# Kernel tuning notes

Hardware: AMD Instinct MI355X
Metric: run time of the kernel (lower is better)

The kernel has to match this reference:

```python
import jax, jax.numpy as jnp
import numpy as np

N_HEAD = 16


def setup_inputs() -> dict:
    key = jax.random.key(0)
    k0, k1, k2, k3 = jax.random.split(key, 4)
    B, T, C = 2, 2048, 1024
    scale = 0.02
    x = jax.random.normal(k0, (B, T, C), dtype=jnp.float32)
    W_attn = jax.random.normal(k1, (C, 3 * C), dtype=jnp.float32) * scale
    b_attn = jnp.zeros((3 * C,), dtype=jnp.float32)
    W_proj = jax.random.normal(k2, (C, C), dtype=jnp.float32) * scale
    b_proj = jnp.zeros((C,), dtype=jnp.float32)
    return {"x": x, "W_attn": W_attn, "b_attn": b_attn, "W_proj": W_proj, "b_proj": b_proj}


def reference(x, W_attn, b_attn, W_proj, b_proj):
    B, T, C = x.shape
    H = N_HEAD
    hd = C // H
    # fused qkv projection
    qkv = x @ W_attn + b_attn                      # [B, T, 3C]
    q, k, v = jnp.split(qkv, 3, axis=-1)
    q = q.reshape(B, T, H, hd).transpose(0, 2, 1, 3)  # [B, H, T, hd]
    k = k.reshape(B, T, H, hd).transpose(0, 2, 1, 3)
    v = v.reshape(B, T, H, hd).transpose(0, 2, 1, 3)
    # scaled dot-product attention with causal mask (past_kv=None -> seq_len == T)
    att = jnp.einsum('bhqd,bhkd->bhqk', q, k) / jnp.sqrt(jnp.float32(hd))
    causal = jnp.tril(jnp.ones((T, T), dtype=bool))  # [T, T]
    att = jnp.where(causal[None, None, :, :], att, jnp.float32(-jnp.inf))
    att = jax.nn.softmax(att, axis=-1)
    y = jnp.einsum('bhqk,bhkd->bhqd', att, v)        # [B, H, T, hd]
    y = y.transpose(0, 2, 1, 3).reshape(B, T, C)
    y = y @ W_proj + b_proj
    return (y, k, v)  # (output, present_k, present_v)
```

## Files before the change

kernel.cpp:

```cpp
#include <hip/hip_runtime.h>
#include <hip/hip_bf16.h>

typedef __bf16 bf16;
typedef __bf16 bf16x8 __attribute__((ext_vector_type(8)));
typedef float f32x4 __attribute__((ext_vector_type(4)));

#define MFMA_BF16(a, b, c) __builtin_amdgcn_mfma_f32_16x16x32_bf16((a), (b), (c), 0, 0, 0)

#define SEQ_T 2048
#define DIM_C 1024

__device__ inline bf16x8 cvt8(const float* p) {
  const f32x4 a = *(const f32x4*)p;
  const f32x4 b = *(const f32x4*)(p + 4);
  bf16x8 r;
  r[0] = (bf16)a[0]; r[1] = (bf16)a[1]; r[2] = (bf16)a[2]; r[3] = (bf16)a[3];
  r[4] = (bf16)b[0]; r[5] = (bf16)b[1]; r[6] = (bf16)b[2]; r[7] = (bf16)b[3];
  return r;
}

template <int MODE, typename AT>
__global__ __launch_bounds__(256) void gemm_kernel(
    const AT* __restrict__ A, const float* __restrict__ W,
    const float* __restrict__ bias, float* __restrict__ out0,
    float* __restrict__ out1, bf16* __restrict__ bq, bf16* __restrict__ bk2,
    int M, int N, int K) {
  __shared__ bf16 As[128][40];
  __shared__ bf16 Bt[128][40];

  const int tid = threadIdx.x;
  const int wid = tid >> 6, lane = tid & 63;
  const int quad = lane >> 4, l16 = lane & 15;
  const int wm = (wid >> 1) * 64, wn = (wid & 1) * 64;
  const int m0 = blockIdx.y * 128, n0 = blockIdx.x * 128;

  const f32x4 zero = {0.f, 0.f, 0.f, 0.f};
  f32x4 acc[4][4];
#pragma unroll
  for (int i = 0; i < 4; i++)
#pragma unroll
    for (int j = 0; j < 4; j++) acc[i][j] = zero;

  for (int kk = 0; kk < K; kk += 32) {
    bf16x8 av[2], wv[2];
#pragma unroll
    for (int p = 0; p < 2; p++) {
      const int s = tid + 256 * p;
      const int ar = s >> 2, aks = s & 3;
      const AT* ap = A + (size_t)(m0 + ar) * K + kk + aks * 8;
      if constexpr (sizeof(AT) == 4) {
        av[p] = cvt8((const float*)ap);
      } else {
        av[p] = *(const bf16x8*)ap;
      }
      const int bn = s & 127, bks = s >> 7;
#pragma unroll
      for (int j = 0; j < 8; j++)
        wv[p][j] = (bf16)W[(size_t)(kk + bks * 8 + j) * N + n0 + bn];
    }
    __syncthreads();
#pragma unroll
    for (int p = 0; p < 2; p++) {
      const int s = tid + 256 * p;
      const int ar = s >> 2, aks = s & 3;
      *(bf16x8*)&As[ar][aks * 8] = av[p];
      const int bn = s & 127, bks = s >> 7;
      *(bf16x8*)&Bt[bn][bks * 8] = wv[p];
    }
    __syncthreads();
    bf16x8 af[4], bfr[4];
#pragma unroll
    for (int i = 0; i < 4; i++)
      af[i] = *(const bf16x8*)&As[wm + i * 16 + l16][quad * 8];
#pragma unroll
    for (int j = 0; j < 4; j++)
      bfr[j] = *(const bf16x8*)&Bt[wn + j * 16 + l16][quad * 8];
#pragma unroll
    for (int i = 0; i < 4; i++)
#pragma unroll
      for (int j = 0; j < 4; j++)
        acc[i][j] = MFMA_BF16(af[i], bfr[j], acc[i][j]);
  }

#pragma unroll
  for (int i = 0; i < 4; i++) {
#pragma unroll
    for (int j = 0; j < 4; j++) {
      const int col = n0 + wn + j * 16 + l16;
      const float bv = bias[col];
#pragma unroll
      for (int r = 0; r < 4; r++) {
        const int gm = m0 + wm + i * 16 + quad * 4 + r;
        const float v = acc[i][j][r] + bv;
        if (MODE == 0) {
          out0[(size_t)gm * N + col] = v;
        } else {
          const int which = col >> 10, c = col & 1023;
          const int h = c >> 6, d = c & 63;
          const int b = gm >> 11, t = gm & (SEQ_T - 1);
          const size_t idx = ((size_t)(b * 16 + h) * SEQ_T + t) * 64 + d;
          if (which == 0) {
            bq[idx] = (bf16)v;
          } else if (which == 1) {
            out0[idx] = v;
            bk2[idx] = (bf16)v;
          } else {
            out1[idx] = v;
          }
        }
      }
    }
  }
}

__global__ __launch_bounds__(512) void attn_kernel(
    const bf16* __restrict__ Qbf, const bf16* __restrict__ Kbf,
    const float* __restrict__ V, bf16* __restrict__ Y) {
  __shared__ bf16 Ks[2][64 * 72];
  __shared__ bf16 Vt[2][64 * 72];
  __shared__ bf16 Ps[8 * 16 * 72];

  const int tid = threadIdx.x;
  const int wid = tid >> 6, lane = tid & 63;
  const int quad = lane >> 4, l16 = lane & 15;

  const int qt = (blockIdx.y < 16) ? ((int)gridDim.x - 1 - (int)blockIdx.x)
                                   : (int)blockIdx.x;
  const int bh = blockIdx.y;
  const int q0 = qt * 128;
  const int b = bh >> 4, h = bh & 15;

  const bf16* qp = Qbf + (size_t)bh * SEQ_T * 64;
  const bf16* kp = Kbf + (size_t)bh * SEQ_T * 64;
  const float* vp = V + (size_t)bh * SEQ_T * 64;

  bf16x8 aq[2];
#pragma unroll
  for (int ks = 0; ks < 2; ks++)
    aq[ks] = *(const bf16x8*)(qp + (size_t)(q0 + wid * 16 + l16) * 64 + ks * 32 + quad * 8);

  bf16x8 bones;
#pragma unroll
  for (int j = 0; j < 8; j++) bones[j] = (bf16)1.0f;

  const f32x4 zero = {0.f, 0.f, 0.f, 0.f};
  f32x4 oacc[4], lacc;
  lacc = zero;
#pragma unroll
  for (int t = 0; t < 4; t++) oacc[t] = zero;

  const int last = 2 * qt + 1;
  bf16x8 kreg;
  f32x4 vf[2];

  auto load_tile = [&](int t) {
    const size_t base = (size_t)t * 64 * 64;
    kreg = *(const bf16x8*)(kp + base + (size_t)tid * 8);
    vf[0] = *(const f32x4*)(vp + base + (size_t)tid * 8);
    vf[1] = *(const f32x4*)(vp + base + (size_t)tid * 8 + 4);
  };
  auto stage_tile = [&](int buf) {
    const int key = tid >> 3, hs = tid & 7;
    *(bf16x8*)&Ks[buf][key * 72 + hs * 8] = kreg;
#pragma unroll
    for (int e = 0; e < 8; e++) {
      const float v = (e < 4) ? vf[0][e] : vf[1][e - 4];
      const int hr = hs * 8 + e;
      Vt[buf][hr * 72 + (((key >> 3) ^ hs) * 8) + (key & 7)] = (bf16)v;
    }
  };

  load_tile(0);
  stage_tile(0);
  load_tile(1);

  for (int it = 0; it <= last; ++it) {
    const int cur = it & 1;
    __syncthreads();
    if (it < last) stage_tile(cur ^ 1);
    if (it + 1 < last) load_tile(it + 2);

    const bool skip = (it == last) && (wid < 4);
    const bool dm = (it == 2 * qt && wid < 4) || (it == last && wid >= 4);

    f32x4 sa[4];
    if (!skip) {
#pragma unroll
      for (int nt = 0; nt < 4; nt++) {
        const bf16x8 bk0 = *(const bf16x8*)&Ks[cur][(nt * 16 + l16) * 72 + quad * 8];
        const bf16x8 bk1 = *(const bf16x8*)&Ks[cur][(nt * 16 + l16) * 72 + 32 + quad * 8];
        f32x4 s = MFMA_BF16(aq[0], bk0, zero);
        s = MFMA_BF16(aq[1], bk1, s);
        sa[nt] = s * 0.125f;
      }
      if (dm) {
#pragma unroll
        for (int nt = 0; nt < 4; nt++) {
          const int col = it * 64 + nt * 16 + l16;
#pragma unroll
          for (int r = 0; r < 4; r++) {
            const int row = q0 + wid * 16 + quad * 4 + r;
            if (col > row) sa[nt][r] = -1e30f;
          }
        }
      }
      bf16* pwb = &Ps[wid * 16 * 72];
#pragma unroll
      for (int nt = 0; nt < 4; nt++) {
        const int cb = nt * 16 + l16;
#pragma unroll
        for (int r = 0; r < 4; r++) {
          const int pr = quad * 4 + r;
          pwb[pr * 72 + (((cb >> 3) ^ (pr & 7)) * 8) + (cb & 7)] = (bf16)__expf(sa[nt][r]);
        }
      }
      bf16x8 ap[2];
#pragma unroll
      for (int ks = 0; ks < 2; ks++)
        ap[ks] = *(const bf16x8*)&pwb[l16 * 72 + (((ks * 4 + quad) ^ (l16 & 7)) * 8)];
      lacc = MFMA_BF16(ap[0], bones, lacc);
      lacc = MFMA_BF16(ap[1], bones, lacc);
#pragma unroll
      for (int nt = 0; nt < 4; nt++) {
        const int n = nt * 16 + l16;
#pragma unroll
        for (int ks = 0; ks < 2; ks++) {
          const bf16x8 bv = *(const bf16x8*)&Vt[cur][n * 72 + (((ks * 4 + quad) ^ (n >> 3)) * 8)];
          oacc[nt] = MFMA_BF16(ap[ks], bv, oacc[nt]);
        }
      }
    }
  }

  float inv[4];
#pragma unroll
  for (int r = 0; r < 4; r++) inv[r] = 1.f / lacc[r];
#pragma unroll
  for (int nt = 0; nt < 4; nt++) {
#pragma unroll
    for (int r = 0; r < 4; r++) {
      const int row = q0 + wid * 16 + quad * 4 + r;
      const int col = h * 64 + nt * 16 + l16;
      Y[((size_t)(b * SEQ_T + row)) * DIM_C + col] = (bf16)(oacc[nt][r] * inv[r]);
    }
  }
}

extern "C" void kernel_launch(void* const* d_in, const int* in_sizes, int n_in,
                              void* d_out, int out_size, void* d_ws, size_t ws_size,
                              hipStream_t stream) {
  (void)in_sizes; (void)n_in; (void)out_size; (void)d_ws; (void)ws_size;
  const float* x = (const float*)d_in[0];
  const float* W_attn = (const float*)d_in[1];
  const float* b_attn = (const float*)d_in[2];
  const float* W_proj = (const float*)d_in[3];
  const float* b_proj = (const float*)d_in[4];

  float* out = (float*)d_out;
  float* y_out = out;
  float* k_out = out + (size_t)4194304;
  float* v_out = out + (size_t)8388608;
  bf16* qbf = (bf16*)d_out;
  bf16* kbf = (bf16*)d_out + 4194304;
  bf16* y_att = (bf16*)d_in[0];

  gemm_kernel<1, float><<<dim3(3072 / 128, 4096 / 128), 256, 0, stream>>>(
      x, W_attn, b_attn, k_out, v_out, qbf, kbf, 4096, 3072, 1024);
  attn_kernel<<<dim3(SEQ_T / 128, 32), 512, 0, stream>>>(qbf, kbf, v_out, y_att);
  gemm_kernel<0, bf16><<<dim3(1024 / 128, 4096 / 128), 256, 0, stream>>>(
      y_att, W_proj, b_proj, y_out, nullptr, nullptr, nullptr, 4096, 1024, 1024);
}
```

Before: 221.3 us.

## Pre-convert inputs and weights to bf16 packed layout; shrink proj GEMM tile

Adds a prep kernel that converts x to bf16 and repacks both weight matrices into k-group-of-8 bf16 layout in workspace. The GEMMs can then load A and W tiles with single 16-byte vector loads instead of scalar strided fp32 loads with in-loop conversion. The output projection GEMM now uses a 64-row M tile, giving more blocks for the smaller N=1024 problem. This costs one extra launch and a full pass over x and the weights every call.

```diff
diff --git a/kernel.cpp b/kernel.cpp
--- a/kernel.cpp
+++ b/kernel.cpp
@@ -10,80 +10,104 @@
 #define SEQ_T 2048
 #define DIM_C 1024
 
-__device__ inline bf16x8 cvt8(const float* p) {
-  const f32x4 a = *(const f32x4*)p;
-  const f32x4 b = *(const f32x4*)(p + 4);
-  bf16x8 r;
-  r[0] = (bf16)a[0]; r[1] = (bf16)a[1]; r[2] = (bf16)a[2]; r[3] = (bf16)a[3];
-  r[4] = (bf16)b[0]; r[5] = (bf16)b[1]; r[6] = (bf16)b[2]; r[7] = (bf16)b[3];
-  return r;
+__global__ __launch_bounds__(256) void prep_kernel(
+    const float* __restrict__ x, const float* __restrict__ Wa,
+    const float* __restrict__ Wp, bf16* __restrict__ xbf,
+    bf16* __restrict__ wat, bf16* __restrict__ wpt) {
+  const int tid = threadIdx.x;
+  const int bid = blockIdx.x;
+  if (bid < 2048) {
+    const size_t i = ((size_t)bid * 256 + tid) * 8;
+    const f32x4 a = *(const f32x4*)(x + i);
+    const f32x4 b = *(const f32x4*)(x + i + 4);
+    bf16x8 r;
+    r[0] = (bf16)a[0]; r[1] = (bf16)a[1]; r[2] = (bf16)a[2]; r[3] = (bf16)a[3];
+    r[4] = (bf16)b[0]; r[5] = (bf16)b[1]; r[6] = (bf16)b[2]; r[7] = (bf16)b[3];
+    *(bf16x8*)(xbf + i) = r;
+  } else if (bid < 3584) {
+    const int cid = (bid - 2048) * 256 + tid;
+    const int kg = cid / 3072, n = cid - kg * 3072;
+    bf16x8 r;
+#pragma unroll
+    for (int j = 0; j < 8; j++) r[j] = (bf16)Wa[(size_t)(kg * 8 + j) * 3072 + n];
+    *(bf16x8*)(wat + (size_t)cid * 8) = r;
+  } else {
+    const int cid = (bid - 3584) * 256 + tid;
+    const int kg = cid >> 10, n = cid & 1023;
+    bf16x8 r;
+#pragma unroll
+    for (int j = 0; j < 8; j++) r[j] = (bf16)Wp[(size_t)(kg * 8 + j) * 1024 + n];
+    *(bf16x8*)(wpt + (size_t)cid * 8) = r;
+  }
 }
 
-template <int MODE, typename AT>
+template <int MODE, int BM>
 __global__ __launch_bounds__(256) void gemm_kernel(
-    const AT* __restrict__ A, const float* __restrict__ W,
+    const bf16* __restrict__ A, const bf16* __restrict__ Wt,
     const float* __restrict__ bias, float* __restrict__ out0,
     float* __restrict__ out1, bf16* __restrict__ bq, bf16* __restrict__ bk2,
     int M, int N, int K) {
-  __shared__ bf16 As[128][40];
+  constexpr int MI = BM / 32;
+  __shared__ bf16 As[BM][40];
   __shared__ bf16 Bt[128][40];
 
   const int tid = threadIdx.x;
   const int wid = tid >> 6, lane = tid & 63;
   const int quad = lane >> 4, l16 = lane & 15;
-  const int wm = (wid >> 1) * 64, wn = (wid & 1) * 64;
-  const int m0 = blockIdx.y * 128, n0 = blockIdx.x * 128;
+  const int wm = (wid >> 1) * (BM / 2), wn = (wid & 1) * 64;
+  const int m0 = blockIdx.y * BM, n0 = blockIdx.x * 128;
 
   const f32x4 zero = {0.f, 0.f, 0.f, 0.f};
-  f32x4 acc[4][4];
-#pragma unroll
-  for (int i = 0; i < 4; i++)
+  f32x4 acc[MI][4];
+#pragma unroll
+  for (int i = 0; i < MI; i++)
 #pragma unroll
     for (int j = 0; j < 4; j++) acc[i][j] = zero;
 
   for (int kk = 0; kk < K; kk += 32) {
-    bf16x8 av[2], wv[2];
+    bf16x8 av[BM / 64], wv[2];
+#pragma unroll
+    for (int p = 0; p < BM / 64; p++) {
+      const int s = tid + 256 * p;
+      const int ar = s >> 2, aks = s & 3;
+      av[p] = *(const bf16x8*)(A + (size_t)(m0 + ar) * K + kk + aks * 8);
+    }
 #pragma unroll
     for (int p = 0; p < 2; p++) {
       const int s = tid + 256 * p;
-      const int ar = s >> 2, aks = s & 3;
-      const AT* ap = A + (size_t)(m0 + ar) * K + kk + aks * 8;
-      if constexpr (sizeof(AT) == 4) {
-        av[p] = cvt8((const float*)ap);
-      } else {
-        av[p] = *(const bf16x8*)ap;
-      }
       const int bn = s & 127, bks = s >> 7;
-#pragma unroll
-      for (int j = 0; j < 8; j++)
-        wv[p][j] = (bf16)W[(size_t)(kk + bks * 8 + j) * N + n0 + bn];
+      wv[p] = *(const bf16x8*)(Wt + ((size_t)((kk >> 3) + bks) * N + n0 + bn) * 8);
     }
     __syncthreads();
 #pragma unroll
-    for (int p = 0; p < 2; p++) {
+    for (int p = 0; p < BM / 64; p++) {
       const int s = tid + 256 * p;
       const int ar = s >> 2, aks = s & 3;
       *(bf16x8*)&As[ar][aks * 8] = av[p];
+    }
+#pragma unroll
+    for (int p = 0; p < 2; p++) {
+      const int s = tid + 256 * p;
       const int bn = s & 127, bks = s >> 7;
       *(bf16x8*)&Bt[bn][bks * 8] = wv[p];
     }
     __syncthreads();
-    bf16x8 af[4], bfr[4];
-#pragma unroll
-    for (int i = 0; i < 4; i++)
+    bf16x8 af[MI], bfr[4];
+#pragma unroll
+    for (int i = 0; i < MI; i++)
       af[i] = *(const bf16x8*)&As[wm + i * 16 + l16][quad * 8];
 #pragma unroll
     for (int j = 0; j < 4; j++)
       bfr[j] = *(const bf16x8*)&Bt[wn + j * 16 + l16][quad * 8];
 #pragma unroll
-    for (int i = 0; i < 4; i++)
+    for (int i = 0; i < MI; i++)
 #pragma unroll
       for (int j = 0; j < 4; j++)
         acc[i][j] = MFMA_BF16(af[i], bfr[j], acc[i][j]);
   }
 
 #pragma unroll
-  for (int i = 0; i < 4; i++) {
+  for (int i = 0; i < MI; i++) {
 #pragma unroll
     for (int j = 0; j < 4; j++) {
       const int col = n0 + wn + j * 16 + l16;
@@ -249,7 +273,7 @@
 extern "C" void kernel_launch(void* const* d_in, const int* in_sizes, int n_in,
                               void* d_out, int out_size, void* d_ws, size_t ws_size,
                               hipStream_t stream) {
-  (void)in_sizes; (void)n_in; (void)out_size; (void)d_ws; (void)ws_size;
+  (void)in_sizes; (void)n_in; (void)out_size; (void)ws_size;
   const float* x = (const float*)d_in[0];
   const float* W_attn = (const float*)d_in[1];
   const float* b_attn = (const float*)d_in[2];
@@ -263,10 +287,14 @@
   bf16* qbf = (bf16*)d_out;
   bf16* kbf = (bf16*)d_out + 4194304;
   bf16* y_att = (bf16*)d_in[0];
-
-  gemm_kernel<1, float><<<dim3(3072 / 128, 4096 / 128), 256, 0, stream>>>(
-      x, W_attn, b_attn, k_out, v_out, qbf, kbf, 4096, 3072, 1024);
+  bf16* xbf = (bf16*)d_ws;
+  bf16* wat = xbf + 4194304;
+  bf16* wpt = wat + 3145728;
+
+  prep_kernel<<<4096, 256, 0, stream>>>(x, W_attn, W_proj, xbf, wat, wpt);
+  gemm_kernel<1, 128><<<dim3(3072 / 128, 4096 / 128), 256, 0, stream>>>(
+      xbf, wat, b_attn, k_out, v_out, qbf, kbf, 4096, 3072, 1024);
   attn_kernel<<<dim3(SEQ_T / 128, 32), 512, 0, stream>>>(qbf, kbf, v_out, y_att);
-  gemm_kernel<0, bf16><<<dim3(1024 / 128, 4096 / 128), 256, 0, stream>>>(
-      y_att, W_proj, b_proj, y_out, nullptr, nullptr, nullptr, 4096, 1024, 1024);
+  gemm_kernel<0, 64><<<dim3(1024 / 128, 4096 / 64), 256, 0, stream>>>(
+      y_att, wpt, b_proj, y_out, nullptr, nullptr, nullptr, 4096, 1024, 1024);
 }
```

Measured after the change: 193.8 us. 1.14x faster.
